# Kernel optimization log

Measured on AMD Instinct MI355X. Metric: run time of the kernel, lower is better.

The kernel has to match this reference:

```python
import jax, jax.numpy as jnp
import numpy as np

B, TE, TD, HE, HD = 8, 256, 128, 512, 512


def setup_inputs() -> dict:
    key = jax.random.key(0)
    k1, k2, k3, k4, k5 = jax.random.split(key, 5)
    # scale weights down (original uses 'uniform' init) to keep tanh unsaturated
    return {
        "encoder_out_seq": jax.random.normal(k1, (B, TE, HE), dtype=jnp.float32),
        "decoder_out_seq": jax.random.normal(k2, (B, TD, HD), dtype=jnp.float32),
        "W_a": jax.random.normal(k3, (HE, HE), dtype=jnp.float32) * 0.05,
        "U_a": jax.random.normal(k4, (HD, HE), dtype=jnp.float32) * 0.05,
        "V_a": jax.random.normal(k5, (HE, 1), dtype=jnp.float32) * 0.05,
    }


def reference(encoder_out_seq, decoder_out_seq, W_a, U_a, V_a):
    # Bahdanau additive attention, vectorized over all decoder timesteps
    # (the original loops over Td via K.rnn; steps are independent).
    Ws = jnp.einsum('bte,eh->bth', encoder_out_seq, W_a)   # [B, Te, He]
    Uh = jnp.einsum('bdk,kh->bdh', decoder_out_seq, U_a)   # [B, Td, He]
    # tanh(S.Wa + h.Ua): broadcast to [B, Td, Te, He], contract with V_a
    act = jnp.tanh(Ws[:, None, :, :] + Uh[:, :, None, :])  # [B, Td, Te, He]
    e = jnp.einsum('bdth,ho->bdt', act, V_a)                # [B, Td, Te]
    e = jax.nn.softmax(e, axis=-1)                          # attention weights
    c = jnp.einsum('bdt,bth->bdh', e, encoder_out_seq)      # [B, Td, He] contexts
    return (c, e)
```

## Files before the change

### kernel.cpp

```cpp
#include <hip/hip_runtime.h>

#define B_  8
#define TE_ 256
#define TD_ 128
#define HE_ 512

typedef __attribute__((ext_vector_type(8))) short short8v;
typedef __attribute__((ext_vector_type(4))) float f32x4;

__global__ __launch_bounds__(512) void gemm_fused(
    const float* __restrict__ enc, const float* __restrict__ dec,
    const float* __restrict__ Wa, const float* __restrict__ Ua,
    float* __restrict__ C) {
  __shared__ short BT[2][32][512];
  const int bid = blockIdx.x;
  const int mt = bid % 24, nt = bid / 24;
  const int m0 = mt * 128, n0 = nt * 32;
  const float* Bsrc = (mt < 16) ? Wa : Ua;
  const float* Asrc = (mt < 16) ? enc + (size_t)m0 * 512
                                : dec + (size_t)(m0 - 2048) * 512;
  const int tid = threadIdx.x;
  {
    const int kr = tid >> 3;
    const int c4 = (tid & 7) * 4;
    for (int p = 0; p < 8; ++p) {
      const int k = kr + p * 64;
      float4 v = *(const float4*)(Bsrc + (size_t)k * 512 + n0 + c4);
      const float vf[4] = {v.x, v.y, v.z, v.w};
      const int kc = k >> 3, klo = k & 7;
#pragma unroll
      for (int q = 0; q < 4; ++q) {
        const int n = c4 + q;
        unsigned u = __float_as_uint(vf[q]);
        unsigned hb = u & 0xffff0000u;
        float lo = vf[q] - __uint_as_float(hb);
        const int slot = (kc & ~7) | ((kc ^ n) & 7);
        BT[0][n][slot * 8 + klo] = (short)(hb >> 16);
        BT[1][n][slot * 8 + klo] = (short)(__float_as_uint(lo) >> 16);
      }
    }
  }
  __syncthreads();
  const int w = tid >> 6, lane = tid & 63;
  const int fm = lane & 15, fc = lane >> 4;
  const float* Ap = Asrc + (size_t)(w * 16 + fm) * 512 + fc * 8;
  f32x4 acc0 = {}, acc1 = {};
  float4 fa = *(const float4*)(Ap);
  float4 fb = *(const float4*)(Ap + 4);
  for (int it = 0; it < 16; ++it) {
    float4 na, nb;
    if (it < 15) {
      na = *(const float4*)(Ap + (it + 1) * 32);
      nb = *(const float4*)(Ap + (it + 1) * 32 + 4);
    }
    const float af[8] = {fa.x, fa.y, fa.z, fa.w, fb.x, fb.y, fb.z, fb.w};
    short8v ah, al;
#pragma unroll
    for (int e = 0; e < 8; ++e) {
      unsigned u = __float_as_uint(af[e]);
      unsigned hb = u & 0xffff0000u;
      ah[e] = (short)(hb >> 16);
      al[e] = (short)(__float_as_uint(af[e] - __uint_as_float(hb)) >> 16);
    }
    const int kc = it * 4 + fc;
    const int base = kc & ~7;
    const int s0 = (base | ((kc ^ fm) & 7)) * 8;
    const int s1 = (base | ((kc ^ (16 + fm)) & 7)) * 8;
    short8v bh0 = *(const short8v*)&BT[0][fm][s0];
    short8v bl0 = *(const short8v*)&BT[1][fm][s0];
    short8v bh1 = *(const short8v*)&BT[0][16 + fm][s1];
    short8v bl1 = *(const short8v*)&BT[1][16 + fm][s1];
    acc0 = __builtin_amdgcn_mfma_f32_16x16x32_bf16(ah, bh0, acc0, 0, 0, 0);
    acc1 = __builtin_amdgcn_mfma_f32_16x16x32_bf16(ah, bh1, acc1, 0, 0, 0);
    acc0 = __builtin_amdgcn_mfma_f32_16x16x32_bf16(ah, bl0, acc0, 0, 0, 0);
    acc1 = __builtin_amdgcn_mfma_f32_16x16x32_bf16(ah, bl1, acc1, 0, 0, 0);
    acc0 = __builtin_amdgcn_mfma_f32_16x16x32_bf16(al, bh0, acc0, 0, 0, 0);
    acc1 = __builtin_amdgcn_mfma_f32_16x16x32_bf16(al, bh1, acc1, 0, 0, 0);
    fa = na; fb = nb;
  }
  const int row = m0 + w * 16 + fc * 4;
  float* Cp = C + (size_t)row * 512 + n0 + fm;
#pragma unroll
  for (int r = 0; r < 4; ++r) Cp[(size_t)r * 512] = acc0[r];
#pragma unroll
  for (int r = 0; r < 4; ++r) Cp[(size_t)r * 512 + 16] = acc1[r];
}

#define C2 2.8853900817779268f
__global__ __launch_bounds__(512) void attn_fused(
    const float* __restrict__ Ws, const float* __restrict__ Uh,
    const float* __restrict__ Va, const float* __restrict__ enc,
    float* __restrict__ c_out, float* __restrict__ e_out) {
  __shared__ float sUh[4][HE_];
  __shared__ float sV[HE_];
  __shared__ float sE[4][TE_];
  __shared__ float sNorm[4];
  const int tid = threadIdx.x;
  const int b  = blockIdx.x & 7;
  const int d0 = (blockIdx.x >> 3) * 4;
  ((float4*)sUh)[tid] = ((const float4*)(Uh + (size_t)(b * TD_ + d0) * HE_))[tid];
  if (tid < 128) ((float4*)sV)[tid] = ((const float4*)Va)[tid];
  __syncthreads();
  const int lane = tid & 63, w = tid >> 6;
  const int tb = w * 32;
  const int h0 = lane * 8;
  float eU[4][8], vv2[8], sumv = 0.f;
#pragma unroll
  for (int j = 0; j < 8; ++j) {
    const float vj = sV[h0 + j];
    sumv += vj;
    vv2[j] = 2.0f * vj;
#pragma unroll
    for (int d = 0; d < 4; ++d)
      eU[d][j] = __builtin_amdgcn_exp2f(C2 * sUh[d][h0 + j]);
  }
  const float* pw = Ws + ((size_t)b * TE_ + tb) * HE_ + h0;
  float4 a0 = *(const float4*)(pw);
  float4 a1 = *(const float4*)(pw + 4);
  float s0, s1, s2, s3;
#define TELT4(X, J) { \
    float EW = __builtin_amdgcn_exp2f(C2 * (X)); \
    float E0 = EW * eU[0][J], E1 = EW * eU[1][J]; \
    float E2 = EW * eU[2][J], E3 = EW * eU[3][J]; \
    float r0 = __builtin_amdgcn_rcpf(E0 + 1.0f); \
    float r1 = __builtin_amdgcn_rcpf(E1 + 1.0f); \
    float r2 = __builtin_amdgcn_rcpf(E2 + 1.0f); \
    float r3 = __builtin_amdgcn_rcpf(E3 + 1.0f); \
    s0 = fmaf(-vv2[J], r0, s0); s1 = fmaf(-vv2[J], r1, s1); \
    s2 = fmaf(-vv2[J], r2, s2); s3 = fmaf(-vv2[J], r3, s3); }
  for (int ti = 0; ti < 32; ++ti) {
    const float* pn = pw + HE_;
    float4 n0 = *(const float4*)(pn);
    float4 n1 = *(const float4*)(pn + 4);
    s0 = s1 = s2 = s3 = sumv;
    TELT4(a0.x, 0) TELT4(a0.y, 1) TELT4(a0.z, 2) TELT4(a0.w, 3)
    TELT4(a1.x, 4) TELT4(a1.y, 5) TELT4(a1.z, 6) TELT4(a1.w, 7)
#pragma unroll
    for (int off = 32; off; off >>= 1) {
      s0 += __shfl_down(s0, off, 64);
      s1 += __shfl_down(s1, off, 64);
      s2 += __shfl_down(s2, off, 64);
      s3 += __shfl_down(s3, off, 64);
    }
    if (lane == 0) {
      sE[0][tb + ti] = s0; sE[1][tb + ti] = s1;
      sE[2][tb + ti] = s2; sE[3][tb + ti] = s3;
    }
    a0 = n0; a1 = n1;
    pw = pn;
  }
  __syncthreads();
  const int dA = tid >> 8, t = tid & 255;
  const float ex0 = __expf(sE[dA][t]);
  const float ex1 = __expf(sE[2 + dA][t]);
  sE[dA][t] = ex0;
  sE[2 + dA][t] = ex1;
  __syncthreads();
  if (w < 4) {
    float s = sE[w][lane] + sE[w][lane + 64] + sE[w][lane + 128] + sE[w][lane + 192];
#pragma unroll
    for (int off = 32; off; off >>= 1) s += __shfl_down(s, off, 64);
    if (lane == 0) sNorm[w] = 1.0f / s;
  }
  __syncthreads();
  const float w0 = ex0 * sNorm[dA];
  const float w1 = ex1 * sNorm[2 + dA];
  sE[dA][t] = w0;
  sE[2 + dA][t] = w1;
  e_out[(size_t)(b * TD_ + d0 + dA) * TE_ + t] = w0;
  e_out[(size_t)(b * TD_ + d0 + 2 + dA) * TE_ + t] = w1;
  __syncthreads();
  float a0c = 0.f, a1c = 0.f, a2c = 0.f, a3c = 0.f;
  const float* ep = enc + (size_t)b * TE_ * HE_ + tid;
#pragma unroll 4
  for (int tt = 0; tt < TE_; ++tt) {
    const float ev = ep[(size_t)tt * HE_];
    a0c = fmaf(sE[0][tt], ev, a0c);
    a1c = fmaf(sE[1][tt], ev, a1c);
    a2c = fmaf(sE[2][tt], ev, a2c);
    a3c = fmaf(sE[3][tt], ev, a3c);
  }
  float* cp = c_out + (size_t)(b * TD_ + d0) * HE_ + tid;
  cp[0]        = a0c;
  cp[HE_]      = a1c;
  cp[2 * HE_]  = a2c;
  cp[3 * HE_]  = a3c;
}

extern "C" void kernel_launch(void* const* d_in, const int* in_sizes, int n_in,
                              void* d_out, int out_size, void* d_ws, size_t ws_size,
                              hipStream_t stream) {
  const float* enc = (const float*)d_in[0];
  const float* dec = (const float*)d_in[1];
  const float* Wa  = (const float*)d_in[2];
  const float* Ua  = (const float*)d_in[3];
  const float* Va  = (const float*)d_in[4];
  float* c_out = (float*)d_out;
  float* e_out = c_out + (size_t)B_ * TD_ * HE_;
  float* Cws = (float*)d_ws;
  const float* Ws = Cws;
  const float* Uh = Cws + (size_t)2048 * 512;
  gemm_fused<<<384, 512, 0, stream>>>(enc, dec, Wa, Ua, Cws);
  attn_fused<<<256, 512, 0, stream>>>(Ws, Uh, Va, enc, c_out, e_out);
}
```

Before: 128.7 us.

## Pre-split A to bf16 hi/lo in separate pass; double attention block threads

Adds a conversion kernel that splits the encoder/decoder activations into bf16 hi/lo arrays once, so the GEMM no longer redoes the split for every N-tile (12 tiles reread each A row). The GEMM now loads pre-split shorts with a two-deep prefetch. The attention kernel moves to 1024 threads, halving the per-wave score rows and splitting the context accumulation over two thread halves, and simplifies the softmax reduction. The cost is an extra kernel launch plus an extra write and read of the split activations through global memory, and higher register pressure at 1024 threads per block.

Result: slower. 132.4 us (+3.0%).

```diff
diff --git a/kernel.cpp b/kernel.cpp
--- a/kernel.cpp
+++ b/kernel.cpp
@@ -5,11 +5,34 @@
 #define TD_ 128
 #define HE_ 512
 
+typedef __attribute__((ext_vector_type(4))) short short4v;
 typedef __attribute__((ext_vector_type(8))) short short8v;
 typedef __attribute__((ext_vector_type(4))) float f32x4;
 
-__global__ __launch_bounds__(512) void gemm_fused(
+__global__ __launch_bounds__(256) void conv_a(
     const float* __restrict__ enc, const float* __restrict__ dec,
+    short* __restrict__ Ahi, short* __restrict__ Alo) {
+  const int idx = blockIdx.x * 256 + threadIdx.x;
+  const int m = idx >> 7;
+  const int k = (idx & 127) << 2;
+  const float* src = (m < 2048) ? (enc + (size_t)m * 512 + k)
+                                : (dec + (size_t)(m - 2048) * 512 + k);
+  float4 v = *(const float4*)src;
+  const float vf[4] = {v.x, v.y, v.z, v.w};
+  short4v hi, lo;
+#pragma unroll
+  for (int j = 0; j < 4; ++j) {
+    unsigned u = __float_as_uint(vf[j]);
+    unsigned hb = u & 0xffff0000u;
+    hi[j] = (short)(hb >> 16);
+    lo[j] = (short)(__float_as_uint(vf[j] - __uint_as_float(hb)) >> 16);
+  }
+  *(short4v*)(Ahi + (size_t)m * 512 + k) = hi;
+  *(short4v*)(Alo + (size_t)m * 512 + k) = lo;
+}
+
+__global__ __launch_bounds__(512) void gemm(
+    const short* __restrict__ Ahi, const short* __restrict__ Alo,
     const float* __restrict__ Wa, const float* __restrict__ Ua,
     float* __restrict__ C) {
   __shared__ short BT[2][32][512];
@@ -17,8 +40,6 @@
   const int mt = bid % 24, nt = bid / 24;
   const int m0 = mt * 128, n0 = nt * 32;
   const float* Bsrc = (mt < 16) ? Wa : Ua;
-  const float* Asrc = (mt < 16) ? enc + (size_t)m0 * 512
-                                : dec + (size_t)(m0 - 2048) * 512;
   const int tid = threadIdx.x;
   {
     const int kr = tid >> 3;
@@ -43,24 +64,20 @@
   __syncthreads();
   const int w = tid >> 6, lane = tid & 63;
   const int fm = lane & 15, fc = lane >> 4;
-  const float* Ap = Asrc + (size_t)(w * 16 + fm) * 512 + fc * 8;
+  const short* Aph = Ahi + (size_t)(m0 + w * 16 + fm) * 512 + fc * 8;
+  const short* Apl = Alo + (size_t)(m0 + w * 16 + fm) * 512 + fc * 8;
   f32x4 acc0 = {}, acc1 = {};
-  float4 fa = *(const float4*)(Ap);
-  float4 fb = *(const float4*)(Ap + 4);
+  short8v pf_h[2], pf_l[2];
+  pf_h[0] = *(const short8v*)(Aph);
+  pf_l[0] = *(const short8v*)(Apl);
+  pf_h[1] = *(const short8v*)(Aph + 32);
+  pf_l[1] = *(const short8v*)(Apl + 32);
   for (int it = 0; it < 16; ++it) {
-    float4 na, nb;
-    if (it < 15) {
-      na = *(const float4*)(Ap + (it + 1) * 32);
-      nb = *(const float4*)(Ap + (it + 1) * 32 + 4);
-    }
-    const float af[8] = {fa.x, fa.y, fa.z, fa.w, fb.x, fb.y, fb.z, fb.w};
-    short8v ah, al;
-#pragma unroll
-    for (int e = 0; e < 8; ++e) {
-      unsigned u = __float_as_uint(af[e]);
-      unsigned hb = u & 0xffff0000u;
-      ah[e] = (short)(hb >> 16);
-      al[e] = (short)(__float_as_uint(af[e] - __uint_as_float(hb)) >> 16);
+    const short8v ah = pf_h[it & 1];
+    const short8v al = pf_l[it & 1];
+    if (it < 14) {
+      pf_h[it & 1] = *(const short8v*)(Aph + (it + 2) * 32);
+      pf_l[it & 1] = *(const short8v*)(Apl + (it + 2) * 32);
     }
     const int kc = it * 4 + fc;
     const int base = kc & ~7;
@@ -76,7 +93,6 @@
     acc1 = __builtin_amdgcn_mfma_f32_16x16x32_bf16(ah, bl1, acc1, 0, 0, 0);
     acc0 = __builtin_amdgcn_mfma_f32_16x16x32_bf16(al, bh0, acc0, 0, 0, 0);
     acc1 = __builtin_amdgcn_mfma_f32_16x16x32_bf16(al, bh1, acc1, 0, 0, 0);
-    fa = na; fb = nb;
   }
   const int row = m0 + w * 16 + fc * 4;
   float* Cp = C + (size_t)row * 512 + n0 + fm;
@@ -87,22 +103,25 @@
 }
 
 #define C2 2.8853900817779268f
-__global__ __launch_bounds__(512) void attn_fused(
+__global__ __launch_bounds__(1024) void attn_fused(
     const float* __restrict__ Ws, const float* __restrict__ Uh,
     const float* __restrict__ Va, const float* __restrict__ enc,
     float* __restrict__ c_out, float* __restrict__ e_out) {
   __shared__ float sUh[4][HE_];
   __shared__ float sV[HE_];
   __shared__ float sE[4][TE_];
+  __shared__ float sRed[16];
   __shared__ float sNorm[4];
   const int tid = threadIdx.x;
   const int b  = blockIdx.x & 7;
   const int d0 = (blockIdx.x >> 3) * 4;
-  ((float4*)sUh)[tid] = ((const float4*)(Uh + (size_t)(b * TD_ + d0) * HE_))[tid];
-  if (tid < 128) ((float4*)sV)[tid] = ((const float4*)Va)[tid];
+  if (tid < 512)
+    ((float4*)sUh)[tid] = ((const float4*)(Uh + (size_t)(b * TD_ + d0) * HE_))[tid];
+  else if (tid < 640)
+    ((float4*)sV)[tid - 512] = ((const float4*)Va)[tid - 512];
   __syncthreads();
   const int lane = tid & 63, w = tid >> 6;
-  const int tb = w * 32;
+  const int tb = w * 16;
   const int h0 = lane * 8;
   float eU[4][8], vv2[8], sumv = 0.f;
 #pragma unroll
@@ -128,7 +147,7 @@
     float r3 = __builtin_amdgcn_rcpf(E3 + 1.0f); \
     s0 = fmaf(-vv2[J], r0, s0); s1 = fmaf(-vv2[J], r1, s1); \
     s2 = fmaf(-vv2[J], r2, s2); s3 = fmaf(-vv2[J], r3, s3); }
-  for (int ti = 0; ti < 32; ++ti) {
+  for (int ti = 0; ti < 16; ++ti) {
     const float* pn = pw + HE_;
     float4 n0 = *(const float4*)(pn);
     float4 n1 = *(const float4*)(pn + 4);
@@ -151,40 +170,34 @@
   }
   __syncthreads();
   const int dA = tid >> 8, t = tid & 255;
-  const float ex0 = __expf(sE[dA][t]);
-  const float ex1 = __expf(sE[2 + dA][t]);
-  sE[dA][t] = ex0;
-  sE[2 + dA][t] = ex1;
-  __syncthreads();
-  if (w < 4) {
-    float s = sE[w][lane] + sE[w][lane + 64] + sE[w][lane + 128] + sE[w][lane + 192];
-#pragma unroll
-    for (int off = 32; off; off >>= 1) s += __shfl_down(s, off, 64);
-    if (lane == 0) sNorm[w] = 1.0f / s;
-  }
-  __syncthreads();
-  const float w0 = ex0 * sNorm[dA];
-  const float w1 = ex1 * sNorm[2 + dA];
-  sE[dA][t] = w0;
-  sE[2 + dA][t] = w1;
-  e_out[(size_t)(b * TD_ + d0 + dA) * TE_ + t] = w0;
-  e_out[(size_t)(b * TD_ + d0 + 2 + dA) * TE_ + t] = w1;
-  __syncthreads();
-  float a0c = 0.f, a1c = 0.f, a2c = 0.f, a3c = 0.f;
-  const float* ep = enc + (size_t)b * TE_ * HE_ + tid;
+  const float ex = __expf(sE[dA][t]);
+  float sum = ex;
+#pragma unroll
+  for (int off = 32; off; off >>= 1) sum += __shfl_down(sum, off, 64);
+  if (lane == 0) sRed[w] = sum;
+  __syncthreads();
+  if (tid < 4)
+    sNorm[tid] = 1.0f / (sRed[tid * 4] + sRed[tid * 4 + 1] + sRed[tid * 4 + 2] + sRed[tid * 4 + 3]);
+  __syncthreads();
+  const float wgt = ex * sNorm[dA];
+  sE[dA][t] = wgt;
+  e_out[(size_t)(b * TD_ + d0 + dA) * TE_ + t] = wgt;
+  __syncthreads();
+  const int h = tid & 511;
+  const int db = (tid >> 9) * 2;
+  float a0c = 0.f, a1c = 0.f;
+  const float* ep = enc + (size_t)b * TE_ * HE_ + h;
+  const float* e0 = sE[db];
+  const float* e1 = sE[db + 1];
 #pragma unroll 4
   for (int tt = 0; tt < TE_; ++tt) {
     const float ev = ep[(size_t)tt * HE_];
-    a0c = fmaf(sE[0][tt], ev, a0c);
-    a1c = fmaf(sE[1][tt], ev, a1c);
-    a2c = fmaf(sE[2][tt], ev, a2c);
-    a3c = fmaf(sE[3][tt], ev, a3c);
-  }
-  float* cp = c_out + (size_t)(b * TD_ + d0) * HE_ + tid;
-  cp[0]        = a0c;
-  cp[HE_]      = a1c;
-  cp[2 * HE_]  = a2c;
-  cp[3 * HE_]  = a3c;
+    a0c = fmaf(e0[tt], ev, a0c);
+    a1c = fmaf(e1[tt], ev, a1c);
+  }
+  float* cp = c_out + (size_t)(b * TD_ + d0 + db) * HE_ + h;
+  cp[0]   = a0c;
+  cp[HE_] = a1c;
 }
 
 extern "C" void kernel_launch(void* const* d_in, const int* in_sizes, int n_in,
@@ -197,9 +210,13 @@
   const float* Va  = (const float*)d_in[4];
   float* c_out = (float*)d_out;
   float* e_out = c_out + (size_t)B_ * TD_ * HE_;
-  float* Cws = (float*)d_ws;
+  char* ws = (char*)d_ws;
+  float* Cws = (float*)ws;
+  short* Ahi = (short*)(ws + (6u << 20));
+  short* Alo = (short*)(ws + (9u << 20));
   const float* Ws = Cws;
   const float* Uh = Cws + (size_t)2048 * 512;
-  gemm_fused<<<384, 512, 0, stream>>>(enc, dec, Wa, Ua, Cws);
-  attn_fused<<<256, 512, 0, stream>>>(Ws, Uh, Va, enc, c_out, e_out);
-}
+  conv_a<<<1536, 256, 0, stream>>>(enc, dec, Ahi, Alo);
+  gemm<<<384, 512, 0, stream>>>(Ahi, Alo, Wa, Ua, Cws);
+  attn_fused<<<256, 1024, 0, stream>>>(Ws, Uh, Va, enc, c_out, e_out);
+}
```
